# Optimization experiments

Hardware: AMD Instinct MI355X
Metric: run time of the kernel (lower is better)

The kernel has to match this reference:

```python
import jax, jax.numpy as jnp
import numpy as np

B, S, D = 1, 4096, 2048
H, KVH, HD = 16, 4, 128  # heads, kv heads, head_dim
ROPE_BASE = 10000.0


def _rope_cos_sin(position_ids):
    # inv_freq: [HD/2]
    inv_freq = 1.0 / (ROPE_BASE ** (jnp.arange(0, HD, 2, dtype=jnp.float32) / HD))
    # freqs: [B, S, HD/2] -> emb: [B, S, HD] (concat(freqs, freqs))
    freqs = position_ids.astype(jnp.float32)[..., None] * inv_freq
    emb = jnp.concatenate([freqs, freqs], axis=-1)
    # [B, 1, S, HD] to broadcast over heads
    return jnp.cos(emb)[:, None, :, :], jnp.sin(emb)[:, None, :, :]


def _rotate_half(x):
    x1, x2 = x[..., : HD // 2], x[..., HD // 2 :]
    return jnp.concatenate([-x2, x1], axis=-1)


def setup_inputs() -> dict:
    key = jax.random.key(0)
    ks = jax.random.split(key, 5)
    s = 0.02
    return {
        "hidden_states": jax.random.normal(ks[0], (B, S, D), jnp.float32),
        "Wq": jax.random.normal(ks[1], (H * HD, D), jnp.float32) * s,
        "Wk": jax.random.normal(ks[2], (KVH * HD, D), jnp.float32) * s,
        "Wv": jax.random.normal(ks[3], (KVH * HD, D), jnp.float32) * s,
        "Wo": jax.random.normal(ks[4], (D, H * HD), jnp.float32) * s,
        "position_ids": jnp.arange(S, dtype=jnp.int64 if jax.config.jax_enable_x64 else jnp.int32)[None, :].repeat(B, 0),
    }


def reference(hidden_states, Wq, Wk, Wv, Wo, position_ids):
    b, s, _ = hidden_states.shape
    # projections (no bias): [b, s, nheads*hd] -> [b, nh, s, hd]
    q = (hidden_states @ Wq.T).reshape(b, s, H, HD).transpose(0, 2, 1, 3)
    k = (hidden_states @ Wk.T).reshape(b, s, KVH, HD).transpose(0, 2, 1, 3)
    v = (hidden_states @ Wv.T).reshape(b, s, KVH, HD).transpose(0, 2, 1, 3)

    cos, sin = _rope_cos_sin(position_ids)  # [b,1,s,hd]
    q = q * cos + _rotate_half(q) * sin
    k = k * cos + _rotate_half(k) * sin

    # GQA: repeat kv heads (repeat_interleave along head dim)
    n_rep = H // KVH
    k = jnp.repeat(k, n_rep, axis=1)
    v = jnp.repeat(v, n_rep, axis=1)

    # eager quadratic attention with causal mask
    scores = jnp.einsum("bhqd,bhkd->bhqk", q, k) / jnp.sqrt(jnp.float32(HD))
    causal = jnp.tril(jnp.ones((s, s), dtype=bool))
    scores = jnp.where(causal[None, None], scores, jnp.finfo(scores.dtype).min)
    attn = jax.nn.softmax(scores, axis=-1)
    out = jnp.einsum("bhqk,bhkd->bhqd", attn, v)  # [b,h,s,hd]
    out = out.transpose(0, 2, 1, 3).reshape(b, s, H * HD)
    return out @ Wo.T
```

## Files before the change

kernel.cpp:

```cpp
#include <hip/hip_runtime.h>
#include <hip/hip_bf16.h>

constexpr int S   = 4096;
constexpr int D   = 2048;
constexpr int H   = 16;
constexpr int KVH = 4;
constexpr int HD  = 128;

using short8 = __attribute__((ext_vector_type(8))) short;
using f32x4  = __attribute__((ext_vector_type(4))) float;
using f32x16 = __attribute__((ext_vector_type(16))) float;

__device__ inline ushort f2bf(float f) {
  union { float f; unsigned u; } x{f};
  unsigned r = x.u + 0x7FFFu + ((x.u >> 16) & 1u);
  return (ushort)(r >> 16);
}
__device__ inline float bf2f(ushort h) {
  union { unsigned u; float f; } x{(unsigned)h << 16};
  return x.f;
}
__device__ inline unsigned pkbf(float a, float b) {
  union { float f; unsigned u; } xa{a}, xb{b};
  unsigned ra = xa.u + 0x7FFFu + ((xa.u >> 16) & 1u);
  unsigned rb = xb.u + 0x7FFFu + ((xb.u >> 16) & 1u);
#if __has_builtin(__builtin_amdgcn_perm)
  return __builtin_amdgcn_perm(rb, ra, 0x07060302u);
#else
  return (rb & 0xFFFF0000u) | (ra >> 16);
#endif
}
__device__ inline unsigned pkbf_t(float a, float b) {
  union { float f; unsigned u; } xa{a}, xb{b};
#if __has_builtin(__builtin_amdgcn_perm)
  return __builtin_amdgcn_perm(xb.u, xa.u, 0x07060302u);
#else
  return (xb.u & 0xFFFF0000u) | (xa.u >> 16);
#endif
}
__device__ inline float fast_exp2(float x) {
#if __has_builtin(__builtin_amdgcn_exp2f)
  return __builtin_amdgcn_exp2f(x);
#else
  return exp2f(x);
#endif
}

__device__ inline void async_copy16(const ushort* g, ushort* l) {
  __builtin_amdgcn_global_load_lds(
      (const __attribute__((address_space(1))) unsigned int*)g,
      (__attribute__((address_space(3))) unsigned int*)l, 16, 0, 0);
}

constexpr size_t N_HID = (size_t)S * D;
constexpr size_t N_WQ  = (size_t)(H * HD) * D;
constexpr size_t N_WKV = (size_t)(KVH * HD) * D;
constexpr size_t C1_ = N_HID;
constexpr size_t C2_ = C1_ + N_WQ;
constexpr size_t C3_ = C2_ + N_WKV;
constexpr size_t C4_ = C3_ + N_WKV;
constexpr size_t C5_ = C4_ + N_WQ;

__global__ void cvt_all_kernel(const float* __restrict__ hid, const float* __restrict__ wq,
                               const float* __restrict__ wk, const float* __restrict__ wv,
                               const float* __restrict__ wo, ushort* __restrict__ dst) {
  size_t i = (size_t)blockIdx.x * blockDim.x + threadIdx.x;
  size_t off = i * 4;
  if (off >= C5_) return;
  const float* src;
  if      (off < C1_) src = hid + off;
  else if (off < C2_) src = wq + (off - C1_);
  else if (off < C3_) src = wk + (off - C2_);
  else if (off < C4_) src = wv + (off - C3_);
  else                src = wo + (off - C4_);
  float4 f = *(const float4*)src;
  ushort4 o;
  o.x = f2bf(f.x); o.y = f2bf(f.y); o.z = f2bf(f.z); o.w = f2bf(f.w);
  *(ushort4*)&dst[off] = o;
}

template <int OUT_MODE>
__device__ __forceinline__ void gemm_tile(const ushort* __restrict__ A,
                                          const ushort* __restrict__ Bt,
                                          void* __restrict__ Cv,
                                          int M, int N, int K, int bxi, int byi,
                                          ushort* As, ushort* Bs) {
  const int bm = byi * 128;
  const int bn = bxi * 128;
  const int tid  = threadIdx.x;
  const int lane = tid & 63;
  const int w    = tid >> 6;
  const int wr = w >> 1, wc = w & 1;
  const int lm = lane & 15, quad = lane >> 4;

  f32x4 acc[4][4];
#pragma unroll
  for (int i = 0; i < 4; ++i)
#pragma unroll
    for (int j = 0; j < 4; ++j) acc[i][j] = (f32x4){0.f, 0.f, 0.f, 0.f};

  for (int k0 = 0; k0 < K; k0 += 32) {
#pragma unroll
    for (int j = 0; j < 2; ++j) {
      int idx = j * 256 + tid;
      int row = idx >> 2;
      int col = (idx & 3) * 8;
      int ubase = (j * 256 + w * 64) * 8;
      async_copy16(A + (size_t)(bm + row) * K + k0 + col, &As[ubase]);
      async_copy16(Bt + (size_t)(bn + row) * K + k0 + col, &Bs[ubase]);
    }
    __syncthreads();
    short8 af[4], bfr[4];
#pragma unroll
    for (int t = 0; t < 4; ++t) {
      af[t]  = *(const short8*)&As[(wr * 64 + t * 16 + lm) * 32 + quad * 8];
      bfr[t] = *(const short8*)&Bs[(wc * 64 + t * 16 + lm) * 32 + quad * 8];
    }
#pragma unroll
    for (int i = 0; i < 4; ++i)
#pragma unroll
      for (int j = 0; j < 4; ++j)
        acc[i][j] = __builtin_amdgcn_mfma_f32_16x16x32_bf16(af[i], bfr[j], acc[i][j], 0, 0, 0);
    __syncthreads();
  }

#pragma unroll
  for (int i = 0; i < 4; ++i)
#pragma unroll
    for (int j = 0; j < 4; ++j) {
      if (OUT_MODE == 2) {
        int col  = bn + wc * 64 + j * 16 + lm;
        int rowb = bm + wr * 64 + i * 16 + quad * 4;
        ushort4 o4;
        o4.x = f2bf(acc[i][j][0]); o4.y = f2bf(acc[i][j][1]);
        o4.z = f2bf(acc[i][j][2]); o4.w = f2bf(acc[i][j][3]);
        *(ushort4*)&((ushort*)Cv)[(size_t)col * M + rowb] = o4;
      } else {
#pragma unroll
        for (int r = 0; r < 4; ++r) {
          size_t row = bm + wr * 64 + i * 16 + quad * 4 + r;
          size_t col = bn + wc * 64 + j * 16 + lm;
          if (OUT_MODE == 1) ((ushort*)Cv)[row * N + col] = f2bf(acc[i][j][r]);
          else               ((float*)Cv)[row * N + col]  = acc[i][j][r];
        }
      }
    }
}

__global__ __launch_bounds__(256) void gemm_qkv_kernel(const ushort* __restrict__ hb,
                                                       const ushort* __restrict__ wq,
                                                       const ushort* __restrict__ wk,
                                                       const ushort* __restrict__ wv,
                                                       ushort* __restrict__ qb,
                                                       ushort* __restrict__ kb,
                                                       ushort* __restrict__ vtb) {
  __shared__ __align__(16) ushort As[128 * 32];
  __shared__ __align__(16) ushort Bs[128 * 32];
  int bid = blockIdx.x;
  if (bid < 512) {
    gemm_tile<1>(hb, wq, qb, S, H * HD, D, bid & 15, bid >> 4, As, Bs);
  } else if (bid < 640) {
    int b = bid - 512;
    gemm_tile<1>(hb, wk, kb, S, KVH * HD, D, b & 3, b >> 2, As, Bs);
  } else {
    int b = bid - 640;
    gemm_tile<2>(hb, wv, vtb, S, KVH * HD, D, b & 3, b >> 2, As, Bs);
  }
}

template <int OUT_MODE>
__global__ __launch_bounds__(256) void gemm_bt_kernel(const ushort* __restrict__ A,
                                                      const ushort* __restrict__ Bt,
                                                      void* __restrict__ Cv,
                                                      int M, int N, int K) {
  __shared__ __align__(16) ushort As[128 * 32];
  __shared__ __align__(16) ushort Bs[128 * 32];
  gemm_tile<OUT_MODE>(A, Bt, Cv, M, N, K, blockIdx.x, blockIdx.y, As, Bs);
}

__global__ void rope_bf16_kernel(ushort* __restrict__ qb, ushort* __restrict__ kb,
                                 const int* __restrict__ pos_ids) {
  int idx = blockIdx.x * blockDim.x + threadIdx.x;
  const int total = S * (H + KVH) * (HD / 2);
  if (idx >= total) return;
  int j = idx & 63;
  int t = idx >> 6;
  int head = t % (H + KVH);
  int s = t / (H + KVH);
  float p = (float)pos_ids[s];
  float inv_freq = exp2f(-(float)j * (13.287712379549449f / 64.0f));
  float ang = p * inv_freq;
  float c = cosf(ang), sn = sinf(ang);
  ushort* base = (head < H) ? (qb + (size_t)s * (H * HD) + head * HD)
                            : (kb + (size_t)s * (KVH * HD) + (head - H) * HD);
  float x1 = bf2f(base[j]), x2 = bf2f(base[j + 64]);
  base[j]      = f2bf(x1 * c - x2 * sn);
  base[j + 64] = f2bf(x2 * c + x1 * sn);
}

template <int SPLIT>
__global__ __launch_bounds__(512) void attn_mfma_kernel(const ushort* __restrict__ q,
                                                        const ushort* __restrict__ k,
                                                        const ushort* __restrict__ Vt,
                                                        ushort* __restrict__ o,
                                                        float* __restrict__ Olo,
                                                        float* __restrict__ Ohi,
                                                        float* __restrict__ Ls) {
  const int bid = blockIdx.x;
  const int h   = 2 * (bid & 7) + ((bid >> 3) & 1);
  const int half = SPLIT ? ((bid >> 4) & 1) : 0;
  const int qi  = SPLIT ? (31 - (bid >> 5)) : (31 - (bid >> 4));
  const int q0  = qi * 128;
  const int kvh = h >> 2;
  const int tid  = threadIdx.x;
  const int lane = tid & 63;
  const int w    = tid >> 6;
  const int qw   = w >> 1;
  const int ks   = w & 1;
  const int m32  = lane & 31;
  const int p    = lane >> 5;

  __shared__ __align__(16) ushort LDSu[32768];

  const int q0w = q0 + qw * 32;

  short8 qf[8];
#pragma unroll
  for (int s = 0; s < 8; ++s)
    qf[s] = *(const short8*)&q[(size_t)(q0w + m32) * (H * HD) + h * HD + s * 16 + p * 8];

  f32x16 Oacc[4];
#pragma unroll
  for (int i = 0; i < 4; ++i)
#pragma unroll
    for (int r = 0; r < 16; ++r) Oacc[i][r] = 0.f;
  float ls4[4] = {0.f, 0.f, 0.f, 0.f};

  auto stage = [&](int k0s, int buf) {
#pragma unroll
    for (int i = 0; i < 4; ++i) {
      int c = w * 4 + i;
      if (c < 16) {
        int kh = c >> 3, s = c & 7;
        async_copy16(&k[(size_t)(k0s + kh * 32 + m32) * (KVH * HD) + kvh * HD + s * 16 + p * 8],
                     &LDSu[buf * 8192 + c * 512]);
      } else {
        int cv = c - 16;
        int ht = cv >> 2, t2 = cv & 3;
        async_copy16(&Vt[(size_t)(kvh * HD + ht * 32 + m32) * S + k0s + t2 * 16 + p * 8],
                     &LDSu[16384 + buf * 8192 + cv * 512]);
      }
    }
  };

  const int T    = SPLIT ? (qi + 1) : (2 * qi + 2);
  const int koff = SPLIT ? (half * (qi + 1)) : 0;

  stage(koff * 64, 0);
  __syncthreads();

  const float C1  = 0.08838834764831845f * 1.4426950408889634f;
  const float F2n = -12.0f * 1.4426950408889634f;

  for (int tt = 0; tt < T; ++tt) {
    const int k0  = (koff + tt) * 64;
    const int cur = tt & 1;
    if (tt + 1 < T) stage(k0 + 64, cur ^ 1);
    const ushort* Kb = &LDSu[cur * 8192];
    const ushort* Vb = &LDSu[16384 + cur * 8192];

    const int kbase = k0 + ks * 32;
    if (kbase <= q0w + 31) {
      f32x16 stA, stB;
#pragma unroll
      for (int r = 0; r < 16; ++r) { stA[r] = 0.f; stB[r] = 0.f; }
#pragma unroll
      for (int s = 0; s < 8; s += 2) {
        short8 kf0 = *(const short8*)&Kb[(ks * 8 + s) * 512 + lane * 8];
        short8 kf1 = *(const short8*)&Kb[(ks * 8 + s + 1) * 512 + lane * 8];
        stA = __builtin_amdgcn_mfma_f32_32x32x16_bf16(kf0, qf[s], stA, 0, 0, 0);
        stB = __builtin_amdgcn_mfma_f32_32x32x16_bf16(kf1, qf[s + 1], stB, 0, 0, 0);
      }

      float pv[16];
      if (kbase == q0w) {
#pragma unroll
        for (int r = 0; r < 16; ++r) {
          int kvl = (r & 3) + 8 * (r >> 2) + 4 * p;
          float e = fast_exp2(fmaf(stA[r] + stB[r], C1, F2n));
          e = (kvl > m32) ? 0.f : e;
          pv[r] = e; ls4[r & 3] += e;
        }
      } else {
#pragma unroll
        for (int r = 0; r < 16; ++r) {
          float e = fast_exp2(fmaf(stA[r] + stB[r], C1, F2n));
          pv[r] = e; ls4[r & 3] += e;
        }
      }

      unsigned own2[4][2], oth[4][2];
#pragma unroll
      for (int g = 0; g < 4; ++g) {
        own2[g][0] = pkbf_t(pv[4 * g + 0], pv[4 * g + 1]);
        own2[g][1] = pkbf_t(pv[4 * g + 2], pv[4 * g + 3]);
        oth[g][0]  = __shfl_xor(own2[g][0], 32);
        oth[g][1]  = __shfl_xor(own2[g][1], 32);
      }
      short8 pf[2];
#pragma unroll
      for (int t2 = 0; t2 < 2; ++t2) {
        union { unsigned u4[4]; short8 s8; } pb;
        pb.u4[0] = p ? oth[2 * t2 + 1][0] : own2[2 * t2][0];
        pb.u4[1] = p ? oth[2 * t2 + 1][1] : own2[2 * t2][1];
        pb.u4[2] = p ? own2[2 * t2 + 1][0] : oth[2 * t2][0];
        pb.u4[3] = p ? own2[2 * t2 + 1][1] : oth[2 * t2][1];
        pf[t2] = pb.s8;
      }

#pragma unroll
      for (int ht = 0; ht < 4; ++ht)
#pragma unroll
        for (int t2l = 0; t2l < 2; ++t2l) {
          int cv = ht * 4 + ks * 2 + t2l;
          short8 vf = *(const short8*)&Vb[cv * 512 + lane * 8];
          Oacc[ht] = __builtin_amdgcn_mfma_f32_32x32x16_bf16(vf, pf[t2l], Oacc[ht], 0, 0, 0);
        }
    }
    __syncthreads();
  }

  float lsum = (ls4[0] + ls4[1]) + (ls4[2] + ls4[3]);
  float* mb = (float*)LDSu;

  if (ks) mb[(qw << 6) | lane] = lsum;
  __syncthreads();
  if (!ks) lsum += mb[(qw << 6) | lane];
  __syncthreads();

  if (ks) {
    float* base = mb + qw * 4096;
#pragma unroll
    for (int ht = 0; ht < 4; ++ht)
#pragma unroll
      for (int r = 0; r < 16; ++r)
        base[ht * 1024 + r * 64 + lane] = Oacc[ht][r];
  }
  __syncthreads();

  if (!ks) {
    const float* base = mb + qw * 4096;
#pragma unroll
    for (int ht = 0; ht < 4; ++ht)
#pragma unroll
      for (int r = 0; r < 16; ++r)
        Oacc[ht][r] += base[ht * 1024 + r * 64 + lane];

    float ltot = lsum + __shfl_xor(lsum, 32);
    if (SPLIT) {
      float* Od = half ? Ohi : Olo;
      size_t rb = (size_t)(q0w + m32) * (H * HD) + h * HD;
#pragma unroll
      for (int ht = 0; ht < 4; ++ht)
#pragma unroll
        for (int rq = 0; rq < 4; ++rq) {
          float4 v;
          v.x = Oacc[ht][4 * rq + 0]; v.y = Oacc[ht][4 * rq + 1];
          v.z = Oacc[ht][4 * rq + 2]; v.w = Oacc[ht][4 * rq + 3];
          *(float4*)&Od[rb + ht * 32 + 8 * rq + 4 * p] = v;
        }
      if (lane < 32) Ls[(size_t)(half * 16 + h) * S + q0w + m32] = ltot;
    } else {
      float inv = 1.0f / ltot;
#pragma unroll
      for (int ht = 0; ht < 4; ++ht)
#pragma unroll
        for (int rq = 0; rq < 4; ++rq) {
          uint2 dd;
          dd.x = pkbf(Oacc[ht][4 * rq + 0] * inv, Oacc[ht][4 * rq + 1] * inv);
          dd.y = pkbf(Oacc[ht][4 * rq + 2] * inv, Oacc[ht][4 * rq + 3] * inv);
          *(uint2*)&o[(size_t)(q0w + m32) * (H * HD) + h * HD + ht * 32 + 8 * rq + 4 * p] = dd;
        }
    }
  }
}

__global__ __launch_bounds__(256) void attn_merge_kernel(const float* __restrict__ Olo,
                                                         const float* __restrict__ Ohi,
                                                         const float* __restrict__ Ls,
                                                         ushort* __restrict__ ob) {
  size_t i4 = ((size_t)blockIdx.x * 256 + threadIdx.x) * 4;
  int s = (int)(i4 >> 11);
  int h = ((int)i4 & 2047) >> 7;
  float inv = 1.0f / (Ls[(size_t)h * S + s] + Ls[(size_t)(16 + h) * S + s]);
  float4 a = *(const float4*)&Olo[i4];
  float4 b = *(const float4*)&Ohi[i4];
  uint2 dd;
  dd.x = pkbf((a.x + b.x) * inv, (a.y + b.y) * inv);
  dd.y = pkbf((a.z + b.z) * inv, (a.w + b.w) * inv);
  *(uint2*)&ob[i4] = dd;
}

extern "C" void kernel_launch(void* const* d_in, const int* in_sizes, int n_in,
                              void* d_out, int out_size, void* d_ws, size_t ws_size,
                              hipStream_t stream) {
  const float* hidden = (const float*)d_in[0];
  const float* Wq     = (const float*)d_in[1];
  const float* Wk     = (const float*)d_in[2];
  const float* Wv     = (const float*)d_in[3];
  const float* Wo     = (const float*)d_in[4];
  const int*   pos    = (const int*)d_in[5];
  float* out = (float*)d_out;

  ushort* hb  = (ushort*)d_ws;
  ushort* wqb = hb  + N_HID;
  ushort* wkb = wqb + N_WQ;
  ushort* wvb = wkb + N_WKV;
  ushort* wob = wvb + N_WKV;
  ushort* qb  = wob + N_WQ;
  ushort* kb  = qb  + (size_t)S * (H * HD);
  ushort* vtb = kb  + (size_t)S * (KVH * HD);
  ushort* ob  = vtb + (size_t)(KVH * HD) * S;
  float* Olo = (float*)d_out;
  float* Ohi = (float*)(ob + (size_t)S * (H * HD));
  float* Ls  = Ohi + (size_t)S * (H * HD);
  size_t ws_need = (size_t)((char*)(Ls + (size_t)2 * H * S) - (char*)d_ws);
  bool split = ws_size >= ws_need;

  dim3 blk(256);
  size_t n4 = C5_ / 4;
  cvt_all_kernel<<<(int)((n4 + 255) / 256), blk, 0, stream>>>(hidden, Wq, Wk, Wv, Wo, hb);

  gemm_qkv_kernel<<<dim3(768), blk, 0, stream>>>(hb, wqb, wkb, wvb, qb, kb, vtb);

  int rope_total = S * (H + KVH) * (HD / 2);
  rope_bf16_kernel<<<(rope_total + 255) / 256, blk, 0, stream>>>(qb, kb, pos);

  if (split) {
    attn_mfma_kernel<1><<<dim3(1024), dim3(512), 0, stream>>>(qb, kb, vtb, ob, Olo, Ohi, Ls);
    attn_merge_kernel<<<dim3((int)((size_t)S * H * HD / 4 / 256)), blk, 0, stream>>>(Olo, Ohi, Ls, ob);
  } else {
    attn_mfma_kernel<0><<<dim3(512), dim3(512), 0, stream>>>(qb, kb, vtb, ob, Olo, Ohi, Ls);
  }

  gemm_bt_kernel<0><<<dim3(D / 128, S / 128), blk, 0, stream>>>(ob, wob, out, S, D, D);
}
```

Measured before the change: 372.2 us.

## Drop intra-block KV split in attention, use 32-key tiles and permlane32 swap

The attention kernel moves from 512 threads (two waves per 32-query group, each handling half of a 64-key tile) to 256 threads where each wave processes a full 32-key tile. This removes the end-of-kernel LDS reduction of partial O accumulators and sums, and halves the LDS footprint. The P-fragment rearrangement now uses permlane32_swap where available instead of two shuffles plus selects. The trade-off is twice as many loop iterations, each with its own barrier and async stage, and fewer waves per block to hide latency.

Result: no change. 371.8 us (-0.1%).

```diff
diff --git a/kernel.cpp b/kernel.cpp
--- a/kernel.cpp
+++ b/kernel.cpp
@@ -43,6 +43,19 @@
   return __builtin_amdgcn_exp2f(x);
 #else
   return exp2f(x);
+#endif
+}
+
+__device__ inline void swap_half(unsigned a, unsigned b, unsigned& x, unsigned& y) {
+#if __has_builtin(__builtin_amdgcn_permlane32_swap)
+  using uint2v = __attribute__((ext_vector_type(2))) unsigned;
+  uint2v r = __builtin_amdgcn_permlane32_swap(a, b, false, false);
+  x = r[0]; y = r[1];
+#else
+  unsigned bx = __shfl_xor(b, 32), ax = __shfl_xor(a, 32);
+  int p = (threadIdx.x & 63) >> 5;
+  x = p ? bx : a;
+  y = p ? b : ax;
 #endif
 }
 
@@ -199,7 +212,7 @@
 }
 
 template <int SPLIT>
-__global__ __launch_bounds__(512) void attn_mfma_kernel(const ushort* __restrict__ q,
+__global__ __launch_bounds__(256) void attn_mfma_kernel(const ushort* __restrict__ q,
                                                         const ushort* __restrict__ k,
                                                         const ushort* __restrict__ Vt,
                                                         ushort* __restrict__ o,
@@ -208,21 +221,20 @@
                                                         float* __restrict__ Ls) {
   const int bid = blockIdx.x;
   const int h   = 2 * (bid & 7) + ((bid >> 3) & 1);
-  const int half = SPLIT ? ((bid >> 4) & 1) : 0;
-  const int qi  = SPLIT ? (31 - (bid >> 5)) : (31 - (bid >> 4));
+  const int t   = bid >> 4;
+  const int half = SPLIT ? (t & 1) : 0;
+  const int qi  = SPLIT ? (31 - (t >> 1)) : (31 - t);
   const int q0  = qi * 128;
   const int kvh = h >> 2;
   const int tid  = threadIdx.x;
   const int lane = tid & 63;
   const int w    = tid >> 6;
-  const int qw   = w >> 1;
-  const int ks   = w & 1;
   const int m32  = lane & 31;
   const int p    = lane >> 5;
 
-  __shared__ __align__(16) ushort LDSu[32768];
-
-  const int q0w = q0 + qw * 32;
+  __shared__ __align__(16) ushort LDSu[16384];
+
+  const int q0w = q0 + w * 32;
 
   short8 qf[8];
 #pragma unroll
@@ -240,50 +252,47 @@
 #pragma unroll
     for (int i = 0; i < 4; ++i) {
       int c = w * 4 + i;
-      if (c < 16) {
-        int kh = c >> 3, s = c & 7;
-        async_copy16(&k[(size_t)(k0s + kh * 32 + m32) * (KVH * HD) + kvh * HD + s * 16 + p * 8],
+      if (c < 8) {
+        async_copy16(&k[(size_t)(k0s + m32) * (KVH * HD) + kvh * HD + c * 16 + p * 8],
                      &LDSu[buf * 8192 + c * 512]);
       } else {
-        int cv = c - 16;
-        int ht = cv >> 2, t2 = cv & 3;
+        int cv = c - 8, ht = cv >> 1, t2 = cv & 1;
         async_copy16(&Vt[(size_t)(kvh * HD + ht * 32 + m32) * S + k0s + t2 * 16 + p * 8],
-                     &LDSu[16384 + buf * 8192 + cv * 512]);
+                     &LDSu[buf * 8192 + 4096 + cv * 512]);
       }
     }
   };
 
-  const int T    = SPLIT ? (qi + 1) : (2 * qi + 2);
-  const int koff = SPLIT ? (half * (qi + 1)) : 0;
-
-  stage(koff * 64, 0);
+  const int T    = SPLIT ? (2 * qi + 2) : (4 * qi + 4);
+  const int koff = SPLIT ? (half * (2 * qi + 2)) : 0;
+
+  stage(koff * 32, 0);
   __syncthreads();
 
   const float C1  = 0.08838834764831845f * 1.4426950408889634f;
   const float F2n = -12.0f * 1.4426950408889634f;
 
   for (int tt = 0; tt < T; ++tt) {
-    const int k0  = (koff + tt) * 64;
+    const int k0  = (koff + tt) * 32;
     const int cur = tt & 1;
-    if (tt + 1 < T) stage(k0 + 64, cur ^ 1);
+    if (tt + 1 < T) stage(k0 + 32, cur ^ 1);
     const ushort* Kb = &LDSu[cur * 8192];
-    const ushort* Vb = &LDSu[16384 + cur * 8192];
-
-    const int kbase = k0 + ks * 32;
-    if (kbase <= q0w + 31) {
+    const ushort* Vb = Kb + 4096;
+
+    if (k0 <= q0w + 31) {
       f32x16 stA, stB;
 #pragma unroll
       for (int r = 0; r < 16; ++r) { stA[r] = 0.f; stB[r] = 0.f; }
 #pragma unroll
       for (int s = 0; s < 8; s += 2) {
-        short8 kf0 = *(const short8*)&Kb[(ks * 8 + s) * 512 + lane * 8];
-        short8 kf1 = *(const short8*)&Kb[(ks * 8 + s + 1) * 512 + lane * 8];
+        short8 kf0 = *(const short8*)&Kb[s * 512 + lane * 8];
+        short8 kf1 = *(const short8*)&Kb[(s + 1) * 512 + lane * 8];
         stA = __builtin_amdgcn_mfma_f32_32x32x16_bf16(kf0, qf[s], stA, 0, 0, 0);
         stB = __builtin_amdgcn_mfma_f32_32x32x16_bf16(kf1, qf[s + 1], stB, 0, 0, 0);
       }
 
       float pv[16];
-      if (kbase == q0w) {
+      if (k0 == q0w) {
 #pragma unroll
         for (int r = 0; r < 16; ++r) {
           int kvl = (r & 3) + 8 * (r >> 2) + 4 * p;
@@ -299,22 +308,20 @@
         }
       }
 
-      unsigned own2[4][2], oth[4][2];
+      unsigned own2[4][2];
 #pragma unroll
       for (int g = 0; g < 4; ++g) {
         own2[g][0] = pkbf_t(pv[4 * g + 0], pv[4 * g + 1]);
         own2[g][1] = pkbf_t(pv[4 * g + 2], pv[4 * g + 3]);
-        oth[g][0]  = __shfl_xor(own2[g][0], 32);
-        oth[g][1]  = __shfl_xor(own2[g][1], 32);
       }
       short8 pf[2];
 #pragma unroll
       for (int t2 = 0; t2 < 2; ++t2) {
+        unsigned x0, y0, x1, y1;
+        swap_half(own2[2 * t2][0], own2[2 * t2 + 1][0], x0, y0);
+        swap_half(own2[2 * t2][1], own2[2 * t2 + 1][1], x1, y1);
         union { unsigned u4[4]; short8 s8; } pb;
-        pb.u4[0] = p ? oth[2 * t2 + 1][0] : own2[2 * t2][0];
-        pb.u4[1] = p ? oth[2 * t2 + 1][1] : own2[2 * t2][1];
-        pb.u4[2] = p ? own2[2 * t2 + 1][0] : oth[2 * t2][0];
-        pb.u4[3] = p ? own2[2 * t2 + 1][1] : oth[2 * t2][1];
+        pb.u4[0] = x0; pb.u4[1] = x1; pb.u4[2] = y0; pb.u4[3] = y1;
         pf[t2] = pb.s8;
       }
 
@@ -322,8 +329,7 @@
       for (int ht = 0; ht < 4; ++ht)
 #pragma unroll
         for (int t2l = 0; t2l < 2; ++t2l) {
-          int cv = ht * 4 + ks * 2 + t2l;
-          short8 vf = *(const short8*)&Vb[cv * 512 + lane * 8];
+          short8 vf = *(const short8*)&Vb[(ht * 2 + t2l) * 512 + lane * 8];
           Oacc[ht] = __builtin_amdgcn_mfma_f32_32x32x16_bf16(vf, pf[t2l], Oacc[ht], 0, 0, 0);
         }
     }
@@ -331,57 +337,32 @@
   }
 
   float lsum = (ls4[0] + ls4[1]) + (ls4[2] + ls4[3]);
-  float* mb = (float*)LDSu;
-
-  if (ks) mb[(qw << 6) | lane] = lsum;
-  __syncthreads();
-  if (!ks) lsum += mb[(qw << 6) | lane];
-  __syncthreads();
-
-  if (ks) {
-    float* base = mb + qw * 4096;
+  float ltot = lsum + __shfl_xor(lsum, 32);
+
+  if (SPLIT) {
+    float* Od = half ? Ohi : Olo;
+    size_t rb = (size_t)(q0w + m32) * (H * HD) + h * HD;
 #pragma unroll
     for (int ht = 0; ht < 4; ++ht)
 #pragma unroll
-      for (int r = 0; r < 16; ++r)
-        base[ht * 1024 + r * 64 + lane] = Oacc[ht][r];
-  }
-  __syncthreads();
-
-  if (!ks) {
-    const float* base = mb + qw * 4096;
+      for (int rq = 0; rq < 4; ++rq) {
+        float4 v;
+        v.x = Oacc[ht][4 * rq + 0]; v.y = Oacc[ht][4 * rq + 1];
+        v.z = Oacc[ht][4 * rq + 2]; v.w = Oacc[ht][4 * rq + 3];
+        *(float4*)&Od[rb + ht * 32 + 8 * rq + 4 * p] = v;
+      }
+    if (lane < 32) Ls[(size_t)(half * 16 + h) * S + q0w + m32] = ltot;
+  } else {
+    float inv = 1.0f / ltot;
 #pragma unroll
     for (int ht = 0; ht < 4; ++ht)
 #pragma unroll
-      for (int r = 0; r < 16; ++r)
-        Oacc[ht][r] += base[ht * 1024 + r * 64 + lane];
-
-    float ltot = lsum + __shfl_xor(lsum, 32);
-    if (SPLIT) {
-      float* Od = half ? Ohi : Olo;
-      size_t rb = (size_t)(q0w + m32) * (H * HD) + h * HD;
-#pragma unroll
-      for (int ht = 0; ht < 4; ++ht)
-#pragma unroll
-        for (int rq = 0; rq < 4; ++rq) {
-          float4 v;
-          v.x = Oacc[ht][4 * rq + 0]; v.y = Oacc[ht][4 * rq + 1];
-          v.z = Oacc[ht][4 * rq + 2]; v.w = Oacc[ht][4 * rq + 3];
-          *(float4*)&Od[rb + ht * 32 + 8 * rq + 4 * p] = v;
-        }
-      if (lane < 32) Ls[(size_t)(half * 16 + h) * S + q0w + m32] = ltot;
-    } else {
-      float inv = 1.0f / ltot;
-#pragma unroll
-      for (int ht = 0; ht < 4; ++ht)
-#pragma unroll
-        for (int rq = 0; rq < 4; ++rq) {
-          uint2 dd;
-          dd.x = pkbf(Oacc[ht][4 * rq + 0] * inv, Oacc[ht][4 * rq + 1] * inv);
-          dd.y = pkbf(Oacc[ht][4 * rq + 2] * inv, Oacc[ht][4 * rq + 3] * inv);
-          *(uint2*)&o[(size_t)(q0w + m32) * (H * HD) + h * HD + ht * 32 + 8 * rq + 4 * p] = dd;
-        }
-    }
+      for (int rq = 0; rq < 4; ++rq) {
+        uint2 dd;
+        dd.x = pkbf(Oacc[ht][4 * rq + 0] * inv, Oacc[ht][4 * rq + 1] * inv);
+        dd.y = pkbf(Oacc[ht][4 * rq + 2] * inv, Oacc[ht][4 * rq + 3] * inv);
+        *(uint2*)&o[(size_t)(q0w + m32) * (H * HD) + h * HD + ht * 32 + 8 * rq + 4 * p] = dd;
+      }
   }
 }
 
@@ -437,10 +418,10 @@
   rope_bf16_kernel<<<(rope_total + 255) / 256, blk, 0, stream>>>(qb, kb, pos);
 
   if (split) {
-    attn_mfma_kernel<1><<<dim3(1024), dim3(512), 0, stream>>>(qb, kb, vtb, ob, Olo, Ohi, Ls);
+    attn_mfma_kernel<1><<<dim3(1024), blk, 0, stream>>>(qb, kb, vtb, ob, Olo, Ohi, Ls);
     attn_merge_kernel<<<dim3((int)((size_t)S * H * HD / 4 / 256)), blk, 0, stream>>>(Olo, Ohi, Ls, ob);
   } else {
-    attn_mfma_kernel<0><<<dim3(512), dim3(512), 0, stream>>>(qb, kb, vtb, ob, Olo, Ohi, Ls);
+    attn_mfma_kernel<0><<<dim3(512), blk, 0, stream>>>(qb, kb, vtb, ob, Olo, Ohi, Ls);
   }
 
   gemm_bt_kernel<0><<<dim3(D / 128, S / 128), blk, 0, stream>>>(ob, wob, out, S, D, D);
```
